# Performance work log

Hardware: AMD Instinct MI355X
Metric: run time of the kernel (lower is better)

## Reference

```python
import jax, jax.numpy as jnp
import numpy as np
from functools import partial

B, T, D = 512, 128, 128
H = 256            # hidden_dim
K = 49             # output_dim (CRF label space)
L = 7              # output_seq_length
LSTM_OUT = 2 * H   # bidirectional


def setup_inputs() -> dict:
    key = jax.random.key(0)
    ks = jax.random.split(key, 16)
    s = 0.1
    inp = {
        'x': jax.random.normal(ks[0], (B, T, D), jnp.float32),
        'labels': jax.random.randint(ks[1], (B, L), 0, K, jnp.int64),
        # LSTM forward direction (gate order i,f,g,o as in PyTorch); biases combined (b_ih+b_hh)
        'w_ih_f': jax.random.normal(ks[2], (4 * H, D), jnp.float32) * s,
        'w_hh_f': jax.random.normal(ks[3], (4 * H, H), jnp.float32) * s,
        'b_f': jax.random.normal(ks[4], (4 * H,), jnp.float32) * s,
        # LSTM backward direction
        'w_ih_b': jax.random.normal(ks[5], (4 * H, D), jnp.float32) * s,
        'w_hh_b': jax.random.normal(ks[6], (4 * H, H), jnp.float32) * s,
        'b_b': jax.random.normal(ks[7], (4 * H,), jnp.float32) * s,
        # attention MLP: Linear(2H -> H) -> tanh -> Linear(H -> 1)
        'aw1': jax.random.normal(ks[8], (H, LSTM_OUT), jnp.float32) * s,
        'ab1': jnp.zeros((H,), jnp.float32),
        'aw2': jax.random.normal(ks[9], (1, H), jnp.float32) * s,
        'ab2': jnp.zeros((1,), jnp.float32),
        # fc: Linear(2H -> K*L)
        'fc_w': jax.random.normal(ks[10], (K * L, LSTM_OUT), jnp.float32) * s,
        'fc_b': jnp.zeros((K * L,), jnp.float32),
        # CRF params
        'start_t': jax.random.normal(ks[11], (K,), jnp.float32) * s,
        'trans': jax.random.normal(ks[12], (K, K), jnp.float32) * s,
        'end_t': jax.random.normal(ks[13], (K,), jnp.float32) * s,
    }
    return inp


def _lstm_dir(x_tbd, w_ih, w_hh, b):
    # x_tbd: [T, B, D] -> hidden states [T, B, H]
    xw = jnp.einsum('tbd,gd->tbg', x_tbd, w_ih) + b  # precompute input projections
    h0 = jnp.zeros((x_tbd.shape[1], w_hh.shape[1]), x_tbd.dtype)
    c0 = jnp.zeros_like(h0)

    def step(carry, xw_t):
        h, c = carry
        gates = xw_t + h @ w_hh.T
        i, f, g, o = jnp.split(gates, 4, axis=-1)
        c = jax.nn.sigmoid(f) * c + jax.nn.sigmoid(i) * jnp.tanh(g)
        h = jax.nn.sigmoid(o) * jnp.tanh(c)
        return (h, c), h

    _, hs = jax.lax.scan(step, (h0, c0), xw)
    return hs


def _crf_loss(em, labels, start_t, trans, end_t):
    # em: [B, L, K]; full mask (all timesteps valid)
    # --- log partition via forward algorithm ---
    alpha0 = start_t + em[:, 0]  # [B, K]

    def step(alpha, em_t):
        alpha = jax.nn.logsumexp(alpha[:, :, None] + trans[None], axis=1) + em_t
        return alpha, None

    alpha, _ = jax.lax.scan(step, alpha0, jnp.swapaxes(em[:, 1:], 0, 1))
    logZ = jax.nn.logsumexp(alpha + end_t, axis=1)  # [B]
    # --- gold path score ---
    em_score = jnp.take_along_axis(em, labels[:, :, None], axis=2).squeeze(-1).sum(axis=1)
    trans_score = trans[labels[:, :-1], labels[:, 1:]].sum(axis=1)
    score = start_t[labels[:, 0]] + em_score + trans_score + end_t[labels[:, -1]]
    return -(score - logZ).mean()


def reference(x, labels, w_ih_f, w_hh_f, b_f, w_ih_b, w_hh_b, b_b,
              aw1, ab1, aw2, ab2, fc_w, fc_b, start_t, trans, end_t):
    labels = labels.astype(jnp.int32)
    x_t = jnp.swapaxes(x, 0, 1)  # [T, B, D]
    h_fwd = _lstm_dir(x_t, w_ih_f, w_hh_f, b_f)                    # [T, B, H]
    h_bwd = _lstm_dir(x_t[::-1], w_ih_b, w_hh_b, b_b)[::-1]        # [T, B, H]
    lstm_out = jnp.swapaxes(jnp.concatenate([h_fwd, h_bwd], axis=-1), 0, 1)  # [B, T, 2H]
    # dropout is identity at inference (eval mode)
    # attention pooling over time
    a = jnp.tanh(jnp.einsum('bte,he->bth', lstm_out, aw1) + ab1)
    scores = jnp.einsum('bth,oh->bto', a, aw2) + ab2               # [B, T, 1]
    attn = jax.nn.softmax(scores, axis=1)
    features = jnp.einsum('bto,bte->be', attn, lstm_out)           # [B, 2H]
    logits = (features @ fc_w.T + fc_b).reshape(-1, L, K)          # emissions [B, L, K]
    return _crf_loss(logits, labels, start_t, trans, end_t)
```

## Files before the change

kernel.cpp:

```cpp
#include <hip/hip_runtime.h>
#include <math.h>

#define B_SZ 512
#define T_SZ 128
#define D_SZ 128
#define H_SZ 256
#define K_SZ 49
#define L_SZ 7
#define E_SZ 512

typedef float f32x4 __attribute__((ext_vector_type(4)));
typedef short bf16x8 __attribute__((ext_vector_type(8)));

__device__ __forceinline__ unsigned short f2bf(float f) {
    union { float f; unsigned u; } v; v.f = f;
    unsigned r = v.u + 0x7FFFu + ((v.u >> 16) & 1u);
    return (unsigned short)(r >> 16);
}
__device__ __forceinline__ float bf2f(unsigned short h) {
    union { unsigned u; float f; } v; v.u = ((unsigned)h) << 16;
    return v.f;
}
__device__ __forceinline__ float fsigm(float x) {
    return __fdividef(1.0f, 1.0f + __expf(-x));
}
__device__ __forceinline__ float ftanh(float x) {
    x = fminf(fmaxf(x, -20.0f), 20.0f);
    float e = __expf(2.0f * x);
    return __fdividef(e - 1.0f, e + 1.0f);
}
__device__ __forceinline__ unsigned char f2fp8(float v) {
    int p = __builtin_amdgcn_cvt_pk_fp8_f32(v, 0.f, 0, false);
    return (unsigned char)(p & 0xff);
}

__global__ __launch_bounds__(256) void prep_w(
    const float* __restrict__ w_ih_f, const float* __restrict__ w_hh_f,
    const float* __restrict__ b_f, const float* __restrict__ w_ih_b,
    const float* __restrict__ w_hh_b, const float* __restrict__ b_b,
    unsigned char* __restrict__ Wt, float* __restrict__ bp)
{
    int idx = blockIdx.x * 256 + threadIdx.x;
    int e  = idx & 7;
    int cu = (idx >> 3) & 127;
    int hi = (idx >> 10) & 3;
    int rest = idx >> 12;
    int kk = rest % 12;
    int dw = rest / 12;
    int wv = dw & 7, dir = dw >> 3;
    int f = cu >> 4, u = cu & 15;
    int q = f >> 2, g = f & 3;
    int j = wv * 32 + q * 16 + u;
    int row = g * H_SZ + j;
    int k = kk * 32 + hi * 8 + e;
    const float* w_ih = dir ? w_ih_b : w_ih_f;
    const float* w_hh = dir ? w_hh_b : w_hh_f;
    float v = (k < H_SZ) ? w_hh[row * H_SZ + k] : w_ih[row * D_SZ + (k - H_SZ)];
    Wt[idx] = f2fp8(v);
    if (kk == 0 && hi == 0 && e == 0)
        bp[dw * 128 + cu] = (dir ? b_b : b_f)[row];
}

__global__ __launch_bounds__(256) void prep_aw(
    const float* __restrict__ aw1, short* __restrict__ aw1b)
{
    int idx = blockIdx.x * 256 + threadIdx.x;
    if (idx < H_SZ * E_SZ) aw1b[idx] = (short)f2bf(aw1[idx]);
}

__global__ __launch_bounds__(256) void xprep(
    const float* __restrict__ x, unsigned char* __restrict__ xb)
{
    size_t i = ((size_t)blockIdx.x * 256 + threadIdx.x) * 4;
    float4 v = *reinterpret_cast<const float4*>(x + i);
    int p0 = __builtin_amdgcn_cvt_pk_fp8_f32(v.x, v.y, 0, false);
    int p1 = __builtin_amdgcn_cvt_pk_fp8_f32(v.z, v.w, 0, false);
    unsigned w = (unsigned)(p0 & 0xffff) | ((unsigned)p1 << 16);
    *reinterpret_cast<unsigned*>(xb + i) = w;
}

__global__ __launch_bounds__(512)
__attribute__((amdgpu_waves_per_eu(2, 2)))
void recur_kernel(
    const unsigned char* __restrict__ xb, const unsigned char* __restrict__ Wt,
    const float* __restrict__ bp, unsigned short* __restrict__ hb)
{
    const int dir = blockIdx.x & 1;
    const int b0 = (blockIdx.x >> 1) * 16;
    const int wv = threadIdx.x >> 6;
    const int l  = threadIdx.x & 63;
    const int u = l & 15, hi = l >> 4;

    __shared__ unsigned char hs[2][16][264];
    __shared__ unsigned char xs[2][16][136];

    for (int i = threadIdx.x; i < 1056; i += 512)
        reinterpret_cast<unsigned*>(&hs[0][0][0])[i] = 0u;

    const int dw = dir * 8 + wv;
    const unsigned char* wb = Wt + (size_t)dw * 49152 + hi * 1024 + u * 8;
    long wreg[12][8];
    #pragma unroll
    for (int kk = 0; kk < 12; ++kk)
        #pragma unroll
        for (int f = 0; f < 8; ++f)
            wreg[kk][f] = *reinterpret_cast<const volatile long*>(wb + kk * 4096 + f * 128);

    float bias[8];
    #pragma unroll
    for (int f = 0; f < 8; ++f)
        bias[f] = bp[dw * 128 + f * 16 + u];

    const int xrow = threadIdx.x >> 5;
    const int xoff = (threadIdx.x & 31) * 4;
    const unsigned char* xbase = xb + (size_t)(b0 + xrow) * T_SZ * D_SZ + xoff;
    const int tstep = dir ? -1 : 1;
    const int t0 = dir ? (T_SZ - 1) : 0;
    *reinterpret_cast<unsigned*>(&xs[0][xrow][xoff]) =
        *reinterpret_cast<const unsigned*>(xbase + (size_t)t0 * D_SZ);
    unsigned xreg = *reinterpret_cast<const unsigned*>(
        xbase + (size_t)(t0 + tstep) * D_SZ);

    float c[2][4] = {};
    int cur = 0;
    __syncthreads();

    for (int s = 0; s < T_SZ; ++s) {
        const int t = dir ? (T_SZ - 1 - s) : s;

        if (s + 1 < T_SZ) {
            *reinterpret_cast<unsigned*>(&xs[(s + 1) & 1][xrow][xoff]) = xreg;
            if (s + 2 < T_SZ)
                xreg = *reinterpret_cast<const unsigned*>(
                    xbase + (size_t)(t + 2 * tstep) * D_SZ);
        }

        f32x4 acc[8];
        #pragma unroll
        for (int f = 0; f < 8; ++f)
            acc[f] = (f32x4){bias[f], bias[f], bias[f], bias[f]};

        #pragma unroll
        for (int kk = 0; kk < 12; ++kk) {
            long a = (kk < 8)
                ? *reinterpret_cast<const long*>(&hs[cur][u][kk * 32 + hi * 8])
                : *reinterpret_cast<const long*>(&xs[s & 1][u][(kk - 8) * 32 + hi * 8]);
            #pragma unroll
            for (int f = 0; f < 8; ++f)
                acc[f] = __builtin_amdgcn_mfma_f32_16x16x32_fp8_fp8(a, wreg[kk][f], acc[f], 0, 0, 0);
        }

        #pragma unroll
        for (int q = 0; q < 2; ++q) {
            const int j = wv * 32 + q * 16 + u;
            #pragma unroll
            for (int r = 0; r < 4; ++r) {
                float iv = fsigm(acc[q * 4 + 0][r]);
                float fv = fsigm(acc[q * 4 + 1][r]);
                float gv = ftanh(acc[q * 4 + 2][r]);
                float ov = fsigm(acc[q * 4 + 3][r]);
                float cn = fv * c[q][r] + iv * gv;
                c[q][r] = cn;
                float h = ov * ftanh(cn);
                int row = hi * 4 + r;
                hs[cur ^ 1][row][j] = f2fp8(h);
                hb[((size_t)t * B_SZ + b0 + row) * E_SZ + dir * H_SZ + j] = f2bf(h);
            }
        }
        __syncthreads();
        cur ^= 1;
    }
}

__global__ __launch_bounds__(256) void attn_mfma(
    const unsigned short* __restrict__ hb, const short* __restrict__ aw1b,
    const float* __restrict__ ab1, const float* __restrict__ aw2,
    float* __restrict__ scores)
{
    const int mt = blockIdx.x >> 1, nt = blockIdx.x & 1;
    const int r0 = mt * 128, n0 = nt * 128;
    const int tid = threadIdx.x;
    const int wv = tid >> 6, l = tid & 63, u = l & 15, hi = l >> 4;
    const int mw = wv >> 1, nw = wv & 1;

    __shared__ unsigned short As[128][40];
    __shared__ unsigned short Bs[128][40];

    f32x4 acc[4][4];
    #pragma unroll
    for (int m = 0; m < 4; ++m)
        #pragma unroll
        for (int n = 0; n < 4; ++n)
            acc[m][n] = (f32x4){0.f, 0.f, 0.f, 0.f};

    const int srow = tid >> 1;
    const int sc0 = (tid & 1) * 16;

    for (int k0 = 0; k0 < E_SZ; k0 += 32) {
        bf16x8 va0 = *reinterpret_cast<const bf16x8*>(hb + (size_t)(r0 + srow) * E_SZ + k0 + sc0);
        bf16x8 va1 = *reinterpret_cast<const bf16x8*>(hb + (size_t)(r0 + srow) * E_SZ + k0 + sc0 + 8);
        bf16x8 vb0 = *reinterpret_cast<const bf16x8*>(aw1b + (size_t)(n0 + srow) * E_SZ + k0 + sc0);
        bf16x8 vb1 = *reinterpret_cast<const bf16x8*>(aw1b + (size_t)(n0 + srow) * E_SZ + k0 + sc0 + 8);
        __syncthreads();
        *reinterpret_cast<bf16x8*>(&As[srow][sc0])     = va0;
        *reinterpret_cast<bf16x8*>(&As[srow][sc0 + 8]) = va1;
        *reinterpret_cast<bf16x8*>(&Bs[srow][sc0])     = vb0;
        *reinterpret_cast<bf16x8*>(&Bs[srow][sc0 + 8]) = vb1;
        __syncthreads();

        bf16x8 af[4], bf[4];
        #pragma unroll
        for (int m = 0; m < 4; ++m)
            af[m] = *reinterpret_cast<const bf16x8*>(&As[mw * 64 + m * 16 + u][hi * 8]);
        #pragma unroll
        for (int n = 0; n < 4; ++n)
            bf[n] = *reinterpret_cast<const bf16x8*>(&Bs[nw * 64 + n * 16 + u][hi * 8]);
        #pragma unroll
        for (int m = 0; m < 4; ++m)
            #pragma unroll
            for (int n = 0; n < 4; ++n)
                acc[m][n] = __builtin_amdgcn_mfma_f32_16x16x32_bf16(af[m], bf[n], acc[m][n], 0, 0, 0);
    }

    float t1[4], t2[4];
    #pragma unroll
    for (int n = 0; n < 4; ++n) {
        int h = n0 + nw * 64 + n * 16 + u;
        t1[n] = ab1[h]; t2[n] = aw2[h];
    }
    #pragma unroll
    for (int m = 0; m < 4; ++m) {
        #pragma unroll
        for (int r = 0; r < 4; ++r) {
            float s = 0.f;
            #pragma unroll
            for (int n = 0; n < 4; ++n)
                s += tanhf(acc[m][n][r] + t1[n]) * t2[n];
            #pragma unroll
            for (int o = 1; o < 16; o <<= 1) s += __shfl_xor(s, o);
            if (u == 0)
                atomicAdd(&scores[r0 + mw * 64 + m * 16 + hi * 4 + r], s);
        }
    }
}

__global__ __launch_bounds__(256) void attn_pool(
    const float* __restrict__ scores, const unsigned short* __restrict__ hb,
    float* __restrict__ features)
{
    int b = blockIdx.x;
    int tid = threadIdx.x;
    __shared__ float w[T_SZ];
    __shared__ float smax[4], ssum[4];

    float sc = (tid < T_SZ) ? scores[(size_t)tid * B_SZ + b] : -INFINITY;
    float m = sc;
    for (int o = 32; o; o >>= 1) m = fmaxf(m, __shfl_xor(m, o));
    if ((tid & 63) == 0) smax[tid >> 6] = m;
    __syncthreads();
    float M = fmaxf(fmaxf(smax[0], smax[1]), fmaxf(smax[2], smax[3]));
    float e = (tid < T_SZ) ? expf(sc - M) : 0.f;
    float se = e;
    for (int o = 32; o; o >>= 1) se += __shfl_xor(se, o);
    if ((tid & 63) == 0) ssum[tid >> 6] = se;
    __syncthreads();
    float S = ssum[0] + ssum[1] + ssum[2] + ssum[3];
    if (tid < T_SZ) w[tid] = e / S;
    __syncthreads();

    for (int e0 = tid; e0 < E_SZ; e0 += 256) {
        float acc = 0.f;
        for (int t = 0; t < T_SZ; ++t)
            acc += w[t] * bf2f(hb[((size_t)t * B_SZ + b) * E_SZ + e0]);
        features[(size_t)b * E_SZ + e0] = acc;
    }
}

__global__ __launch_bounds__(256) void fc_kernel(
    const float* __restrict__ features, const float* __restrict__ fc_w,
    const float* __restrict__ fc_b, float* __restrict__ logits)
{
    int bb = blockIdx.x * 8;
    int tid = threadIdx.x;
    __shared__ float f[8][E_SZ];
    for (int i = tid; i < 8 * E_SZ; i += 256)
        f[i >> 9][i & 511] = features[(size_t)(bb + (i >> 9)) * E_SZ + (i & 511)];
    __syncthreads();
    for (int o = tid; o < K_SZ * L_SZ; o += 256) {
        const float* wr = fc_w + (size_t)o * E_SZ;
        float acc[8];
        float bv = fc_b[o];
        #pragma unroll
        for (int b = 0; b < 8; ++b) acc[b] = bv;
        for (int e0 = 0; e0 < E_SZ; ++e0) {
            float wv = wr[e0];
            #pragma unroll
            for (int b = 0; b < 8; ++b) acc[b] += f[b][e0] * wv;
        }
        #pragma unroll
        for (int b = 0; b < 8; ++b)
            logits[(size_t)(bb + b) * (K_SZ * L_SZ) + o] = acc[b];
    }
}

__global__ __launch_bounds__(64) void crf_kernel(
    const float* __restrict__ logits, const int* __restrict__ labels,
    const float* __restrict__ start_t, const float* __restrict__ trans,
    const float* __restrict__ end_t, float* __restrict__ per_loss)
{
    int b = blockIdx.x;
    int tid = threadIdx.x;
    __shared__ float tr[K_SZ * K_SZ];
    __shared__ float em[K_SZ * L_SZ];
    __shared__ float alpha[K_SZ];

    for (int i = tid; i < K_SZ * K_SZ; i += 64) tr[i] = trans[i];
    for (int i = tid; i < K_SZ * L_SZ; i += 64)
        em[i] = logits[(size_t)b * (K_SZ * L_SZ) + i];
    __syncthreads();
    if (tid < K_SZ) alpha[tid] = start_t[tid] + em[tid];
    __syncthreads();

    for (int t = 1; t < L_SZ; ++t) {
        float na = 0.f;
        if (tid < K_SZ) {
            float m = -INFINITY;
            for (int k = 0; k < K_SZ; ++k)
                m = fmaxf(m, alpha[k] + tr[k * K_SZ + tid]);
            float s = 0.f;
            for (int k = 0; k < K_SZ; ++k)
                s += expf(alpha[k] + tr[k * K_SZ + tid] - m);
            na = m + logf(s) + em[t * K_SZ + tid];
        }
        __syncthreads();
        if (tid < K_SZ) alpha[tid] = na;
        __syncthreads();
    }

    float v = (tid < K_SZ) ? alpha[tid] + end_t[tid] : -INFINITY;
    float m = v;
    for (int o = 32; o; o >>= 1) m = fmaxf(m, __shfl_xor(m, o));
    float e = (tid < K_SZ) ? expf(v - m) : 0.f;
    for (int o = 32; o; o >>= 1) e += __shfl_xor(e, o);
    float logZ = m + logf(e);

    if (tid == 0) {
        const int* lab = labels + (size_t)b * L_SZ;
        float score = start_t[lab[0]] + end_t[lab[L_SZ - 1]];
        for (int t = 0; t < L_SZ; ++t) score += em[t * K_SZ + lab[t]];
        for (int t = 0; t < L_SZ - 1; ++t) score += tr[lab[t] * K_SZ + lab[t + 1]];
        per_loss[b] = logZ - score;
    }
}

__global__ __launch_bounds__(256) void reduce_kernel(
    const float* __restrict__ per_loss, float* __restrict__ out)
{
    int tid = threadIdx.x;
    float s = per_loss[tid] + per_loss[tid + 256];
    for (int o = 32; o; o >>= 1) s += __shfl_xor(s, o);
    __shared__ float part[4];
    if ((tid & 63) == 0) part[tid >> 6] = s;
    __syncthreads();
    if (tid == 0) out[0] = (part[0] + part[1] + part[2] + part[3]) / (float)B_SZ;
}

extern "C" void kernel_launch(void* const* d_in, const int* in_sizes, int n_in,
                              void* d_out, int out_size, void* d_ws, size_t ws_size,
                              hipStream_t stream)
{
    const float* x      = (const float*)d_in[0];
    const int*   labels = (const int*)d_in[1];
    const float* w_ih_f = (const float*)d_in[2];
    const float* w_hh_f = (const float*)d_in[3];
    const float* b_f    = (const float*)d_in[4];
    const float* w_ih_b = (const float*)d_in[5];
    const float* w_hh_b = (const float*)d_in[6];
    const float* b_b    = (const float*)d_in[7];
    const float* aw1    = (const float*)d_in[8];
    const float* ab1    = (const float*)d_in[9];
    const float* aw2    = (const float*)d_in[10];
    const float* fc_w   = (const float*)d_in[12];
    const float* fc_b   = (const float*)d_in[13];
    const float* start_t = (const float*)d_in[14];
    const float* trans   = (const float*)d_in[15];
    const float* end_t   = (const float*)d_in[16];
    float* out = (float*)d_out;

    char* ws = (char*)d_ws;
    size_t off = 0;
    unsigned char* Wt = (unsigned char*)(ws + off); off += (size_t)786432;
    float* bp        = (float*)(ws + off); off += (size_t)2048 * 4;
    short* aw1b      = (short*)(ws + off); off += (size_t)H_SZ * E_SZ * 2;
    unsigned char* xb = (unsigned char*)(ws + off); off += (size_t)B_SZ * T_SZ * D_SZ;
    unsigned short* hb = (unsigned short*)(ws + off); off += (size_t)T_SZ * B_SZ * E_SZ * 2;
    float* scores    = (float*)(ws + off); off += (size_t)T_SZ * B_SZ * 4;
    float* features  = (float*)(ws + off); off += (size_t)B_SZ * E_SZ * 4;
    float* logits    = (float*)(ws + off); off += (size_t)B_SZ * K_SZ * L_SZ * 4;
    float* per_loss  = (float*)(ws + off); off += (size_t)B_SZ * 4;

    prep_w<<<3072, 256, 0, stream>>>(
        w_ih_f, w_hh_f, b_f, w_ih_b, w_hh_b, b_b, Wt, bp);
    prep_aw<<<(H_SZ * E_SZ + 255) / 256, 256, 0, stream>>>(aw1, aw1b);
    xprep<<<(B_SZ * T_SZ * D_SZ / 4 + 255) / 256, 256, 0, stream>>>(x, xb);

    hipMemsetAsync(scores, 0, (size_t)T_SZ * B_SZ * 4, stream);

    recur_kernel<<<64, 512, 0, stream>>>(xb, Wt, bp, hb);

    attn_mfma<<<1024, 256, 0, stream>>>(hb, aw1b, ab1, aw2, scores);

    attn_pool<<<B_SZ, 256, 0, stream>>>(scores, hb, features);

    fc_kernel<<<64, 256, 0, stream>>>(features, fc_w, fc_b, logits);

    crf_kernel<<<B_SZ, 64, 0, stream>>>(logits, labels, start_t, trans, end_t, per_loss);

    reduce_kernel<<<1, 256, 0, stream>>>(per_loss, out);
}
```

Baseline: 978.8 us.

## Keep recurrent weights in AGPRs via inline asm and stage last input slices in LDS

The persistent weight fragments of the LSTM recurrence move into accumulator registers: inline-asm MFMA takes the B operand from AGPRs for the first ten K-slices. The last two input-projection slices are loaded from a new 64 KB LDS buffer each step instead of being held in registers. The aim is to ease VGPR pressure at two waves per EU and avoid spills. The cost is extra LDS traffic and footprint, an inline-asm hazard nop, and reliance on the compiler honouring the AGPR constraint.

```diff
diff --git a/kernel.cpp b/kernel.cpp
--- a/kernel.cpp
+++ b/kernel.cpp
@@ -32,6 +32,12 @@
 __device__ __forceinline__ unsigned char f2fp8(float v) {
     int p = __builtin_amdgcn_cvt_pk_fp8_f32(v, 0.f, 0, false);
     return (unsigned char)(p & 0xff);
+}
+
+__device__ __forceinline__ void mfma_fp8_a(f32x4& acc, long a, long w) {
+    asm volatile("v_mfma_f32_16x16x32_fp8_fp8 %0, %1, %2, %0"
+                 : "+v"(acc)
+                 : "v"(a), "a"(w));
 }
 
 __global__ __launch_bounds__(256) void prep_w(
@@ -93,18 +99,31 @@
 
     __shared__ unsigned char hs[2][16][264];
     __shared__ unsigned char xs[2][16][136];
+    __shared__ long wlds[128][64];
 
     for (int i = threadIdx.x; i < 1056; i += 512)
         reinterpret_cast<unsigned*>(&hs[0][0][0])[i] = 0u;
 
+    for (int i = threadIdx.x; i < 128 * 64; i += 512) {
+        int slabf = i >> 6;
+        int ll = i & 63;
+        int wvv = slabf >> 4;
+        int kkr = (slabf >> 3) & 1;
+        int ff = slabf & 7;
+        int hi2 = ll >> 4, uu = ll & 15;
+        int dww = dir * 8 + wvv;
+        wlds[slabf][ll] = *reinterpret_cast<const long*>(
+            Wt + (((size_t)(dww * 12 + 10 + kkr) * 4 + hi2) * 128 + (ff * 16 + uu)) * 8);
+    }
+
     const int dw = dir * 8 + wv;
     const unsigned char* wb = Wt + (size_t)dw * 49152 + hi * 1024 + u * 8;
-    long wreg[12][8];
+    long wrega[10][8];
     #pragma unroll
-    for (int kk = 0; kk < 12; ++kk)
+    for (int kk = 0; kk < 10; ++kk)
         #pragma unroll
         for (int f = 0; f < 8; ++f)
-            wreg[kk][f] = *reinterpret_cast<const volatile long*>(wb + kk * 4096 + f * 128);
+            wrega[kk][f] = *reinterpret_cast<const volatile long*>(wb + kk * 4096 + f * 128);
 
     float bias[8];
     #pragma unroll
@@ -141,14 +160,28 @@
             acc[f] = (f32x4){bias[f], bias[f], bias[f], bias[f]};
 
         #pragma unroll
-        for (int kk = 0; kk < 12; ++kk) {
-            long a = (kk < 8)
-                ? *reinterpret_cast<const long*>(&hs[cur][u][kk * 32 + hi * 8])
-                : *reinterpret_cast<const long*>(&xs[s & 1][u][(kk - 8) * 32 + hi * 8]);
+        for (int kk = 0; kk < 8; ++kk) {
+            long a = *reinterpret_cast<const long*>(&hs[cur][u][kk * 32 + hi * 8]);
             #pragma unroll
             for (int f = 0; f < 8; ++f)
-                acc[f] = __builtin_amdgcn_mfma_f32_16x16x32_fp8_fp8(a, wreg[kk][f], acc[f], 0, 0, 0);
-        }
+                mfma_fp8_a(acc[f], a, wrega[kk][f]);
+        }
+        #pragma unroll
+        for (int kk = 8; kk < 10; ++kk) {
+            long a = *reinterpret_cast<const long*>(&xs[s & 1][u][(kk - 8) * 32 + hi * 8]);
+            #pragma unroll
+            for (int f = 0; f < 8; ++f)
+                mfma_fp8_a(acc[f], a, wrega[kk][f]);
+        }
+        #pragma unroll
+        for (int kkr = 0; kkr < 2; ++kkr) {
+            long a = *reinterpret_cast<const long*>(&xs[s & 1][u][(2 + kkr) * 32 + hi * 8]);
+            #pragma unroll
+            for (int f = 0; f < 8; ++f)
+                acc[f] = __builtin_amdgcn_mfma_f32_16x16x32_fp8_fp8(
+                    a, wlds[wv * 16 + kkr * 8 + f][l], acc[f], 0, 0, 0);
+        }
+        asm volatile("s_nop 7\n\ts_nop 3" ::);
 
         #pragma unroll
         for (int q = 0; q < 2; ++q) {
```

New measurement: 1.012 ms. 1.03x slower.
